# Kernel tuning notes

Measured on AMD Instinct MI355X. Metric: run time of the kernel, lower is better.

Reference implementation:

```python
import jax, jax.numpy as jnp
import numpy as np

N, E, D_IN, D_HID, D_OUT = 50000, 800000, 64, 128, 64


def setup_inputs() -> dict:
    key = jax.random.key(0)
    ks = jax.random.split(key, 8)
    x = jax.random.normal(ks[0], (N, D_IN), dtype=jnp.float32)
    edge_index = jax.random.randint(ks[1], (2, E), 0, N, dtype=jnp.int64)
    # SAGEConv layer 1: lin_l (agg path, with bias), lin_r (root path, no bias)
    s1 = 1.0 / np.sqrt(D_IN)
    W_l1 = jax.random.uniform(ks[2], (D_HID, D_IN), jnp.float32, -s1, s1)
    b_l1 = jnp.zeros((D_HID,), jnp.float32)
    W_r1 = jax.random.uniform(ks[3], (D_HID, D_IN), jnp.float32, -s1, s1)
    s2 = 1.0 / np.sqrt(D_HID)
    W_l2 = jax.random.uniform(ks[4], (D_OUT, D_HID), jnp.float32, -s2, s2)
    b_l2 = jnp.zeros((D_OUT,), jnp.float32)
    W_r2 = jax.random.uniform(ks[5], (D_OUT, D_HID), jnp.float32, -s2, s2)
    return {"x": x, "edge_index": edge_index,
            "W_l1": W_l1, "b_l1": b_l1, "W_r1": W_r1,
            "W_l2": W_l2, "b_l2": b_l2, "W_r2": W_r2}


def _sage_layer(h, src, dst, W_l, b_l, W_r, n_nodes):
    # scatter-mean of source features onto targets
    msg = h[src]                                               # [E, d]
    summed = jax.ops.segment_sum(msg, dst, num_segments=n_nodes)
    deg = jax.ops.segment_sum(jnp.ones((src.shape[0], 1), h.dtype), dst,
                              num_segments=n_nodes)
    agg = summed / jnp.maximum(deg, 1.0)                       # [n, d]
    return agg @ W_l.T + b_l + h @ W_r.T


def reference(x, edge_index, W_l1, b_l1, W_r1, W_l2, b_l2, W_r2):
    src, dst = edge_index[0], edge_index[1]
    n = x.shape[0]
    h = _sage_layer(x, src, dst, W_l1, b_l1, W_r1, n)
    h = jnp.tanh(h)
    h = _sage_layer(h, src, dst, W_l2, b_l2, W_r2, n)
    return jax.nn.log_softmax(h, axis=1)
```

## Files before the change

kernel.cpp:

```cpp
#include <hip/hip_runtime.h>
#include <hip/hip_bf16.h>
#include <math.h>


typedef unsigned short u16;
typedef unsigned int   u32;
typedef __attribute__((ext_vector_type(8))) __bf16 bf16x8;
typedef __attribute__((ext_vector_type(4))) float  f32x4;

__device__ __forceinline__ u16 f2bf(float f) {
    u32 u = __float_as_uint(f);
    u32 r = (u + 0x7FFFu + ((u >> 16) & 1u)) >> 16;
    return (u16)r;
}
__device__ __forceinline__ float bfl(u32 u) { return __uint_as_float(u << 16); }
__device__ __forceinline__ float bfh(u32 u) { return __uint_as_float(u & 0xFFFF0000u); }
__device__ __forceinline__ u32 pack2(float a, float b) {
    return (u32)f2bf(a) | ((u32)f2bf(b) << 16);
}
__device__ __forceinline__ int pad16(int x) { return (x + 15) & ~15; }

__global__ __launch_bounds__(256) void misc_kernel(
    const float* __restrict__ x, uint4* __restrict__ xb4, int nCvt8,
    const float* __restrict__ Wl1, const float* __restrict__ Wr1,
    const float* __restrict__ Wl2, const float* __restrict__ Wr2,
    u16* __restrict__ W1c, u16* __restrict__ W2c,
    u16* __restrict__ perm, int permStore8,
    int* __restrict__ cnt, int nCnt4,
    u16* __restrict__ xb, u16* __restrict__ m2b,
    int N, int VB, int PB, int ZB)
{
    int blk = blockIdx.x, tid = threadIdx.x;
    if (blk < VB) {
        int i = blk * 256 + tid;
        if (i < nCvt8) {
            float4 v0 = ((const float4*)x)[i * 2];
            float4 v1 = ((const float4*)x)[i * 2 + 1];
            uint4 p;
            p.x = pack2(v0.x, v0.y); p.y = pack2(v0.z, v0.w);
            p.z = pack2(v1.x, v1.y); p.w = pack2(v1.z, v1.w);
            xb4[i] = p;
        }
    } else if (blk < VB + 64) {
        int i = (blk - VB) * 256 + tid;
        if (i < 128 * 128) {
            int o = i >> 7, k = i & 127;
            float w1 = (k < 64) ? Wr1[o * 64 + k] : Wl1[o * 64 + (k - 64)];
            W1c[i] = f2bf(w1);
            float w2 = (o < 64) ? Wl2[o * 128 + k] : Wr2[(o - 64) * 128 + k];
            W2c[i] = f2bf(w2);
        }
    } else if (blk < VB + 64 + PB) {
        int i = (blk - VB - 64) * 256 + tid;
        if (i < permStore8) {
            u32 v = (u32)N | ((u32)N << 16);
            uint4 q; q.x = v; q.y = v; q.z = v; q.w = v;
            ((uint4*)perm)[i] = q;
        }
    } else if (blk < VB + 64 + PB + ZB) {
        int i = (blk - VB - 64 - PB) * 256 + tid;
        if (i < nCnt4) {
            uint4 z; z.x = 0; z.y = 0; z.z = 0; z.w = 0;
            ((uint4*)cnt)[i] = z;
        }
    } else {
        if (tid < 32)      ((u32*)(xb  + (size_t)N * 64))[tid] = 0;
        else if (tid < 64) ((u32*)(m2b + (size_t)N * 64))[tid - 32] = 0;
    }
}

__global__ __launch_bounds__(256) void fill_kernel(
    const int* __restrict__ src, const int* __restrict__ dst,
    int* __restrict__ cnt, u16* __restrict__ perm, int E, int N8, float invN8)
{
    int g = blockIdx.x & 7;
    int e0 = (blockIdx.x >> 3) * 2048 + threadIdx.x * 8;
    int d[8];
    if (e0 + 8 <= E) {
        int4 d0 = *(const int4*)(dst + e0);
        int4 d1 = *(const int4*)(dst + e0 + 4);
        d[0] = d0.x; d[1] = d0.y; d[2] = d0.z; d[3] = d0.w;
        d[4] = d1.x; d[5] = d1.y; d[6] = d1.z; d[7] = d1.w;
    } else {
        for (int k = 0; k < 8; k++) d[k] = (e0 + k < E) ? dst[e0 + k] : -1;
    }
#pragma unroll
    for (int k = 0; k < 8; k++) {
        int dd = d[k];
        if (dd < 0) continue;
        int b = (int)((float)dd * invN8);
        if (dd >= (b + 1) * N8) b++;
        else if (dd < b * N8) b--;
        if (b != g) continue;
        int pos = atomicAdd(&cnt[dd], 1);
        if (pos < 64) perm[(size_t)dd * 64 + pos] = (u16)src[e0 + k];
    }
}

__device__ __forceinline__ void gather_wide(
    const u32* __restrict__ feat2, const u16* __restrict__ perm,
    int slot0, int pd, int rg, int c8, float acc[8])
{
    float accB[8];
#pragma unroll
    for (int k = 0; k < 8; k++) { acc[k] = 0.f; accB[k] = 0.f; }
    int pidx = (int)perm[slot0 + (rg * 8 + c8)];
    for (int j = 0; j < pd; j += 16) {
        int rA = __shfl(pidx, j + rg,     64);
        int rB = __shfl(pidx, j + 8 + rg, 64);
        uint4 uA = *(const uint4*)(feat2 + (size_t)rA * 32 + c8 * 4);
        uint4 uB = *(const uint4*)(feat2 + (size_t)rB * 32 + c8 * 4);
        acc[0] += bfl(uA.x); acc[1] += bfh(uA.x);
        acc[2] += bfl(uA.y); acc[3] += bfh(uA.y);
        acc[4] += bfl(uA.z); acc[5] += bfh(uA.z);
        acc[6] += bfl(uA.w); acc[7] += bfh(uA.w);
        accB[0] += bfl(uB.x); accB[1] += bfh(uB.x);
        accB[2] += bfl(uB.y); accB[3] += bfh(uB.y);
        accB[4] += bfl(uB.z); accB[5] += bfh(uB.z);
        accB[6] += bfl(uB.w); accB[7] += bfh(uB.w);
    }
#pragma unroll
    for (int k = 0; k < 8; k++) acc[k] += accB[k];
#pragma unroll
    for (int k = 0; k < 8; k++) {
        acc[k] += __shfl_xor(acc[k], 8, 64);
        acc[k] += __shfl_xor(acc[k], 16, 64);
        acc[k] += __shfl_xor(acc[k], 32, 64);
    }
}

__global__ __launch_bounds__(256) void gather1_kernel(
    const u32* __restrict__ xb2, const u16* __restrict__ perm,
    const int* __restrict__ cnt, u32* __restrict__ aggb2, int N)
{
    int wid  = blockIdx.x * 4 + (threadIdx.x >> 6);
    int lane = threadIdx.x & 63;
    if (wid >= N) return;
    int deg = cnt[wid];
    int pd = pad16(min(deg, 64));
    int rg = lane >> 3, c8 = lane & 7;
    float acc[8];
    gather_wide(xb2, perm, wid * 64, pd, rg, c8, acc);
    if (rg == 0) {
        float inv = 1.f / fmaxf((float)deg, 1.f);
        uint4 p;
        p.x = pack2(acc[0] * inv, acc[1] * inv);
        p.y = pack2(acc[2] * inv, acc[3] * inv);
        p.z = pack2(acc[4] * inv, acc[5] * inv);
        p.w = pack2(acc[6] * inv, acc[7] * inv);
        *(uint4*)(aggb2 + (size_t)wid * 32 + c8 * 4) = p;
    }
}

__global__ __launch_bounds__(256) void layer12_mfma(
    const u16* __restrict__ xb, const u16* __restrict__ aggb,
    const u16* __restrict__ W1, const float* __restrict__ b1,
    const u16* __restrict__ W2, const float* __restrict__ b2,
    u16* __restrict__ m2b, float* __restrict__ out, int N)
{
    __shared__ u16 tile[4][2048];
    int tid = threadIdx.x;
    int wv = tid >> 6, lane = tid & 63;
    int quad = lane >> 4, l16 = lane & 15;
    int node = blockIdx.x * 64 + wv * 16 + l16;
    int nclamp = min(node, N - 1);
    const u16* xrow = xb   + (size_t)nclamp * 64;
    const u16* arow = aggb + (size_t)nclamp * 64;
    bf16x8 a0 = *(const bf16x8*)(xrow + quad * 8);
    bf16x8 a1 = *(const bf16x8*)(xrow + 32 + quad * 8);
    bf16x8 a2 = *(const bf16x8*)(arow + quad * 8);
    bf16x8 a3 = *(const bf16x8*)(arow + 32 + quad * 8);
#pragma unroll
    for (int nt = 0; nt < 8; nt++) {
        const u16* wrow = W1 + (size_t)(nt * 16 + l16) * 128 + quad * 8;
        f32x4 acc = {0.f, 0.f, 0.f, 0.f};
        acc = __builtin_amdgcn_mfma_f32_16x16x32_bf16(a0, *(const bf16x8*)(wrow),      acc, 0, 0, 0);
        acc = __builtin_amdgcn_mfma_f32_16x16x32_bf16(a1, *(const bf16x8*)(wrow + 32), acc, 0, 0, 0);
        acc = __builtin_amdgcn_mfma_f32_16x16x32_bf16(a2, *(const bf16x8*)(wrow + 64), acc, 0, 0, 0);
        acc = __builtin_amdgcn_mfma_f32_16x16x32_bf16(a3, *(const bf16x8*)(wrow + 96), acc, 0, 0, 0);
        int col = nt * 16 + l16;
        float bias = b1[col];
#pragma unroll
        for (int r = 0; r < 4; r++) {
            int row = quad * 4 + r;
            tile[wv][row * 128 + (col ^ ((row & 7) << 3))] =
                f2bf(tanhf(acc[r] + bias));
        }
    }
    __syncthreads();
    int swz = (l16 & 7) << 3;
    bf16x8 h0 = *(const bf16x8*)&tile[wv][l16 * 128 + (( 0 + quad * 8) ^ swz)];
    bf16x8 h1 = *(const bf16x8*)&tile[wv][l16 * 128 + ((32 + quad * 8) ^ swz)];
    bf16x8 h2 = *(const bf16x8*)&tile[wv][l16 * 128 + ((64 + quad * 8) ^ swz)];
    bf16x8 h3 = *(const bf16x8*)&tile[wv][l16 * 128 + ((96 + quad * 8) ^ swz)];
    int orow = blockIdx.x * 64 + wv * 16 + quad * 4;
#pragma unroll
    for (int nt = 0; nt < 8; nt++) {
        const u16* wrow = W2 + (size_t)(nt * 16 + l16) * 128 + quad * 8;
        f32x4 acc = {0.f, 0.f, 0.f, 0.f};
        acc = __builtin_amdgcn_mfma_f32_16x16x32_bf16(h0, *(const bf16x8*)(wrow),      acc, 0, 0, 0);
        acc = __builtin_amdgcn_mfma_f32_16x16x32_bf16(h1, *(const bf16x8*)(wrow + 32), acc, 0, 0, 0);
        acc = __builtin_amdgcn_mfma_f32_16x16x32_bf16(h2, *(const bf16x8*)(wrow + 64), acc, 0, 0, 0);
        acc = __builtin_amdgcn_mfma_f32_16x16x32_bf16(h3, *(const bf16x8*)(wrow + 96), acc, 0, 0, 0);
        int oc = nt * 16 + l16;
#pragma unroll
        for (int r = 0; r < 4; r++) {
            int nn = orow + r;
            if (nn >= N) continue;
            if (oc < 64) m2b[(size_t)nn * 64 + oc] = f2bf(acc[r]);
            else         out[(size_t)nn * 64 + (oc - 64)] = acc[r] + b2[oc - 64];
        }
    }
}

__global__ __launch_bounds__(256) void gather2_final_kernel(
    const u32* __restrict__ m2b2, const u16* __restrict__ perm,
    const int* __restrict__ cnt, float* __restrict__ out, int N)
{
    int wid  = blockIdx.x * 4 + (threadIdx.x >> 6);
    int lane = threadIdx.x & 63;
    if (wid >= N) return;
    int deg = cnt[wid];
    int pd = pad16(min(deg, 64));
    int rg = lane >> 3, c8 = lane & 7;
    float acc[8];
    gather_wide(m2b2, perm, wid * 64, pd, rg, c8, acc);
    float inv = 1.f / fmaxf((float)deg, 1.f);
    const float4* orow = (const float4*)(out + (size_t)wid * 64);
    float4 r20 = orow[c8 * 2];
    float4 r21 = orow[c8 * 2 + 1];
    float v[8];
    v[0] = acc[0] * inv + r20.x; v[1] = acc[1] * inv + r20.y;
    v[2] = acc[2] * inv + r20.z; v[3] = acc[3] * inv + r20.w;
    v[4] = acc[4] * inv + r21.x; v[5] = acc[5] * inv + r21.y;
    v[6] = acc[6] * inv + r21.z; v[7] = acc[7] * inv + r21.w;
    float m = v[0];
#pragma unroll
    for (int k = 1; k < 8; k++) m = fmaxf(m, v[k]);
#pragma unroll
    for (int o = 1; o < 8; o <<= 1) m = fmaxf(m, __shfl_xor(m, o, 64));
    float s = 0.f;
#pragma unroll
    for (int k = 0; k < 8; k++) s += expf(v[k] - m);
#pragma unroll
    for (int o = 1; o < 8; o <<= 1) s += __shfl_xor(s, o, 64);
    if (rg == 0) {
        float ls = m + logf(s);
        float4* ow = (float4*)(out + (size_t)wid * 64);
        ow[c8 * 2]     = make_float4(v[0] - ls, v[1] - ls, v[2] - ls, v[3] - ls);
        ow[c8 * 2 + 1] = make_float4(v[4] - ls, v[5] - ls, v[6] - ls, v[7] - ls);
    }
}

extern "C" void kernel_launch(void* const* d_in, const int* in_sizes, int n_in,
                              void* d_out, int out_size, void* d_ws, size_t ws_size,
                              hipStream_t stream)
{
    const float* x   = (const float*)d_in[0];
    const int*   ei  = (const int*)d_in[1];
    const float* Wl1 = (const float*)d_in[2];
    const float* bl1 = (const float*)d_in[3];
    const float* Wr1 = (const float*)d_in[4];
    const float* Wl2 = (const float*)d_in[5];
    const float* bl2 = (const float*)d_in[6];
    const float* Wr2 = (const float*)d_in[7];
    float* out = (float*)d_out;

    int N = in_sizes[0] / 64;
    int E = in_sizes[1] / 2;
    const int* src = ei;
    const int* dst = ei + E;
    int N8 = (N + 7) / 8;
    float invN8 = 1.0f / (float)N8;

    size_t permN = (size_t)N * 64;
    int permStore8 = (int)(permN / 8);
    int PB = (permStore8 + 255) / 256;

    char* wsb = (char*)d_ws;
    size_t npad = ((size_t)N + 64) & ~(size_t)63;
    int* cnt  = (int*)wsb;
    u16* perm = (u16*)(cnt + npad);
    u16* xb   = perm + permN;
    u16* aggb = xb + (size_t)(N + 1) * 64;
    u16* m2b  = aggb + (size_t)N * 64;
    u16* W1c  = m2b + (size_t)(N + 1) * 64;
    u16* W2c  = W1c + 128 * 128;

    int nCvt8 = N * 64 / 8;
    int VB = (nCvt8 + 255) / 256;
    int nCnt4 = N / 4;
    int ZB = (nCnt4 + 255) / 256;
    misc_kernel<<<VB + 64 + PB + ZB + 1, 256, 0, stream>>>(
        x, (uint4*)xb, nCvt8,
        Wl1, Wr1, Wl2, Wr2, W1c, W2c,
        perm, permStore8, cnt, nCnt4, xb, m2b, N, VB, PB, ZB);

    {
        int chunks = (E + 2047) / 2048;
        fill_kernel<<<chunks * 8, 256, 0, stream>>>(src, dst, cnt, perm, E,
                                                    N8, invN8);
    }

    gather1_kernel<<<(N + 3) / 4, 256, 0, stream>>>((const u32*)xb, perm,
                                                    cnt, (u32*)aggb, N);

    layer12_mfma<<<(N + 63) / 64, 256, 0, stream>>>(xb, aggb, W1c, bl1,
                                                    W2c, bl2, m2b, out, N);

    gather2_final_kernel<<<(N + 3) / 4, 256, 0, stream>>>((const u32*)m2b, perm,
                                                          cnt, out, N);
}
```

Baseline: 203.6 us.

## Fuse layer-1 gather into MFMA kernel and fold edge fill into prep

The layer-1 neighbor gather now runs inside the dense MFMA kernel. Eight waves gather 64 node rows into a swizzled LDS tile, then four waves run both layer matmuls on it, so the aggregated buffer no longer goes through global memory. The full perm prefill is dropped: lanes beyond a node's degree are masked to the zero sentinel row. The count reset is done with a memset, and the edge bucketing fill shares one launch with the x and weight bf16 conversions. The cost is that half the waves in the fused kernel sit idle during the matmul phase, and the block is larger, which may lower occupancy.

```diff
diff --git a/kernel.cpp b/kernel.cpp
--- a/kernel.cpp
+++ b/kernel.cpp
@@ -20,61 +20,13 @@
 }
 __device__ __forceinline__ int pad16(int x) { return (x + 15) & ~15; }
 
-__global__ __launch_bounds__(256) void misc_kernel(
-    const float* __restrict__ x, uint4* __restrict__ xb4, int nCvt8,
-    const float* __restrict__ Wl1, const float* __restrict__ Wr1,
-    const float* __restrict__ Wl2, const float* __restrict__ Wr2,
-    u16* __restrict__ W1c, u16* __restrict__ W2c,
-    u16* __restrict__ perm, int permStore8,
-    int* __restrict__ cnt, int nCnt4,
-    u16* __restrict__ xb, u16* __restrict__ m2b,
-    int N, int VB, int PB, int ZB)
-{
-    int blk = blockIdx.x, tid = threadIdx.x;
-    if (blk < VB) {
-        int i = blk * 256 + tid;
-        if (i < nCvt8) {
-            float4 v0 = ((const float4*)x)[i * 2];
-            float4 v1 = ((const float4*)x)[i * 2 + 1];
-            uint4 p;
-            p.x = pack2(v0.x, v0.y); p.y = pack2(v0.z, v0.w);
-            p.z = pack2(v1.x, v1.y); p.w = pack2(v1.z, v1.w);
-            xb4[i] = p;
-        }
-    } else if (blk < VB + 64) {
-        int i = (blk - VB) * 256 + tid;
-        if (i < 128 * 128) {
-            int o = i >> 7, k = i & 127;
-            float w1 = (k < 64) ? Wr1[o * 64 + k] : Wl1[o * 64 + (k - 64)];
-            W1c[i] = f2bf(w1);
-            float w2 = (o < 64) ? Wl2[o * 128 + k] : Wr2[(o - 64) * 128 + k];
-            W2c[i] = f2bf(w2);
-        }
-    } else if (blk < VB + 64 + PB) {
-        int i = (blk - VB - 64) * 256 + tid;
-        if (i < permStore8) {
-            u32 v = (u32)N | ((u32)N << 16);
-            uint4 q; q.x = v; q.y = v; q.z = v; q.w = v;
-            ((uint4*)perm)[i] = q;
-        }
-    } else if (blk < VB + 64 + PB + ZB) {
-        int i = (blk - VB - 64 - PB) * 256 + tid;
-        if (i < nCnt4) {
-            uint4 z; z.x = 0; z.y = 0; z.z = 0; z.w = 0;
-            ((uint4*)cnt)[i] = z;
-        }
-    } else {
-        if (tid < 32)      ((u32*)(xb  + (size_t)N * 64))[tid] = 0;
-        else if (tid < 64) ((u32*)(m2b + (size_t)N * 64))[tid - 32] = 0;
-    }
-}
-
-__global__ __launch_bounds__(256) void fill_kernel(
+__device__ __forceinline__ void fill_body(
     const int* __restrict__ src, const int* __restrict__ dst,
-    int* __restrict__ cnt, u16* __restrict__ perm, int E, int N8, float invN8)
-{
-    int g = blockIdx.x & 7;
-    int e0 = (blockIdx.x >> 3) * 2048 + threadIdx.x * 8;
+    int* __restrict__ cnt, u16* __restrict__ perm, int E, int N8,
+    float invN8, int vb, int tid)
+{
+    int g = vb & 7;
+    int e0 = (vb >> 3) * 2048 + tid * 8;
     int d[8];
     if (e0 + 8 <= E) {
         int4 d0 = *(const int4*)(dst + e0);
@@ -97,14 +49,54 @@
     }
 }
 
+__global__ __launch_bounds__(256) void prep_kernel(
+    const int* __restrict__ src, const int* __restrict__ dst,
+    int* __restrict__ cnt, u16* __restrict__ perm, int E, int N8, float invN8,
+    const float* __restrict__ x, uint4* __restrict__ xb4, int nCvt8,
+    const float* __restrict__ Wl1, const float* __restrict__ Wr1,
+    const float* __restrict__ Wl2, const float* __restrict__ Wr2,
+    u16* __restrict__ W1c, u16* __restrict__ W2c,
+    u16* __restrict__ xb, u16* __restrict__ m2b,
+    int N, int FB, int VB)
+{
+    int blk = blockIdx.x, tid = threadIdx.x;
+    if (blk < FB) {
+        fill_body(src, dst, cnt, perm, E, N8, invN8, blk, tid);
+    } else if (blk < FB + VB) {
+        int i = (blk - FB) * 256 + tid;
+        if (i < nCvt8) {
+            float4 v0 = ((const float4*)x)[i * 2];
+            float4 v1 = ((const float4*)x)[i * 2 + 1];
+            uint4 p;
+            p.x = pack2(v0.x, v0.y); p.y = pack2(v0.z, v0.w);
+            p.z = pack2(v1.x, v1.y); p.w = pack2(v1.z, v1.w);
+            xb4[i] = p;
+        }
+    } else if (blk < FB + VB + 64) {
+        int i = (blk - FB - VB) * 256 + tid;
+        if (i < 128 * 128) {
+            int o = i >> 7, k = i & 127;
+            float w1 = (k < 64) ? Wr1[o * 64 + k] : Wl1[o * 64 + (k - 64)];
+            W1c[i] = f2bf(w1);
+            float w2 = (o < 64) ? Wl2[o * 128 + k] : Wr2[(o - 64) * 128 + k];
+            W2c[i] = f2bf(w2);
+        }
+    } else {
+        if (tid < 32)      ((u32*)(xb  + (size_t)N * 64))[tid] = 0;
+        else if (tid < 64) ((u32*)(m2b + (size_t)N * 64))[tid - 32] = 0;
+    }
+}
+
 __device__ __forceinline__ void gather_wide(
     const u32* __restrict__ feat2, const u16* __restrict__ perm,
-    int slot0, int pd, int rg, int c8, float acc[8])
+    int slot0, int degc, int pd, int rg, int c8, int lane, int N,
+    float acc[8])
 {
     float accB[8];
 #pragma unroll
     for (int k = 0; k < 8; k++) { acc[k] = 0.f; accB[k] = 0.f; }
-    int pidx = (int)perm[slot0 + (rg * 8 + c8)];
+    int pidx = (int)perm[slot0 + lane];
+    pidx = (lane < degc) ? pidx : N;
     for (int j = 0; j < pd; j += 16) {
         int rA = __shfl(pidx, j + rg,     64);
         int rB = __shfl(pidx, j + 8 + rg, 64);
@@ -129,102 +121,116 @@
     }
 }
 
-__global__ __launch_bounds__(256) void gather1_kernel(
-    const u32* __restrict__ xb2, const u16* __restrict__ perm,
-    const int* __restrict__ cnt, u32* __restrict__ aggb2, int N)
+__global__ __launch_bounds__(512) void gather_layer12_kernel(
+    const u16* __restrict__ xb, const u16* __restrict__ perm,
+    const int* __restrict__ cnt,
+    const u16* __restrict__ W1, const float* __restrict__ b1,
+    const u16* __restrict__ W2, const float* __restrict__ b2,
+    u16* __restrict__ m2b, float* __restrict__ out, int N)
+{
+    __shared__ u16 agg_lds[64 * 64];
+    __shared__ u16 tile4[4 * 2048];
+    const int tid = threadIdx.x;
+    const int wv = tid >> 6, lane = tid & 63;
+    const int tb = blockIdx.x;
+
+    {
+        const int rg = lane >> 3, c8 = lane & 7;
+#pragma unroll 2
+        for (int i = 0; i < 8; i++) {
+            int rr = wv * 8 + i;
+            int nodec = min(tb * 64 + rr, N - 1);
+            int deg = cnt[nodec];
+            int degc = min(deg, 64);
+            int pd = pad16(degc);
+            float acc[8];
+            gather_wide((const u32*)xb, perm, nodec * 64, degc, pd,
+                        rg, c8, lane, N, acc);
+            if (rg == 0) {
+                float inv = 1.f / fmaxf((float)deg, 1.f);
+                uint4 p;
+                p.x = pack2(acc[0] * inv, acc[1] * inv);
+                p.y = pack2(acc[2] * inv, acc[3] * inv);
+                p.z = pack2(acc[4] * inv, acc[5] * inv);
+                p.w = pack2(acc[6] * inv, acc[7] * inv);
+                *(uint4*)&agg_lds[rr * 64 + ((c8 ^ (rr & 7)) << 3)] = p;
+            }
+        }
+    }
+    __syncthreads();
+
+    const int quad = lane >> 4, l16 = lane & 15;
+    u16* tile = tile4 + wv * 2048;
+    bf16x8 a0, a1, a2, a3;
+    if (wv < 4) {
+        int node = tb * 64 + wv * 16 + l16;
+        int nclamp = min(node, N - 1);
+        const u16* xrow = xb + (size_t)nclamp * 64;
+        a0 = *(const bf16x8*)(xrow + quad * 8);
+        a1 = *(const bf16x8*)(xrow + 32 + quad * 8);
+        int rr = wv * 16 + l16;
+        a2 = *(const bf16x8*)&agg_lds[rr * 64 + ((quad       ^ (rr & 7)) << 3)];
+        a3 = *(const bf16x8*)&agg_lds[rr * 64 + (((quad + 4) ^ (rr & 7)) << 3)];
+#pragma unroll
+        for (int nt = 0; nt < 8; nt++) {
+            const u16* wrow = W1 + (size_t)(nt * 16 + l16) * 128 + quad * 8;
+            f32x4 acc = {0.f, 0.f, 0.f, 0.f};
+            acc = __builtin_amdgcn_mfma_f32_16x16x32_bf16(a0, *(const bf16x8*)(wrow),      acc, 0, 0, 0);
+            acc = __builtin_amdgcn_mfma_f32_16x16x32_bf16(a1, *(const bf16x8*)(wrow + 32), acc, 0, 0, 0);
+            acc = __builtin_amdgcn_mfma_f32_16x16x32_bf16(a2, *(const bf16x8*)(wrow + 64), acc, 0, 0, 0);
+            acc = __builtin_amdgcn_mfma_f32_16x16x32_bf16(a3, *(const bf16x8*)(wrow + 96), acc, 0, 0, 0);
+            int col = nt * 16 + l16;
+            float bias = b1[col];
+#pragma unroll
+            for (int r = 0; r < 4; r++) {
+                int row = quad * 4 + r;
+                tile[row * 128 + (col ^ ((row & 7) << 3))] =
+                    f2bf(tanhf(acc[r] + bias));
+            }
+        }
+    }
+    __syncthreads();
+
+    if (wv < 4) {
+        int swz = (l16 & 7) << 3;
+        bf16x8 h0 = *(const bf16x8*)&tile[l16 * 128 + (( 0 + quad * 8) ^ swz)];
+        bf16x8 h1 = *(const bf16x8*)&tile[l16 * 128 + ((32 + quad * 8) ^ swz)];
+        bf16x8 h2 = *(const bf16x8*)&tile[l16 * 128 + ((64 + quad * 8) ^ swz)];
+        bf16x8 h3 = *(const bf16x8*)&tile[l16 * 128 + ((96 + quad * 8) ^ swz)];
+        int orow = tb * 64 + wv * 16 + quad * 4;
+#pragma unroll
+        for (int nt = 0; nt < 8; nt++) {
+            const u16* wrow = W2 + (size_t)(nt * 16 + l16) * 128 + quad * 8;
+            f32x4 acc = {0.f, 0.f, 0.f, 0.f};
+            acc = __builtin_amdgcn_mfma_f32_16x16x32_bf16(h0, *(const bf16x8*)(wrow),      acc, 0, 0, 0);
+            acc = __builtin_amdgcn_mfma_f32_16x16x32_bf16(h1, *(const bf16x8*)(wrow + 32), acc, 0, 0, 0);
+            acc = __builtin_amdgcn_mfma_f32_16x16x32_bf16(h2, *(const bf16x8*)(wrow + 64), acc, 0, 0, 0);
+            acc = __builtin_amdgcn_mfma_f32_16x16x32_bf16(h3, *(const bf16x8*)(wrow + 96), acc, 0, 0, 0);
+            int oc = nt * 16 + l16;
+#pragma unroll
+            for (int r = 0; r < 4; r++) {
+                int nn = orow + r;
+                if (nn >= N) continue;
+                if (oc < 64) m2b[(size_t)nn * 64 + oc] = f2bf(acc[r]);
+                else         out[(size_t)nn * 64 + (oc - 64)] = acc[r] + b2[oc - 64];
+            }
+        }
+    }
+}
+
+__global__ __launch_bounds__(256) void gather2_final_kernel(
+    const u32* __restrict__ m2b2, const u16* __restrict__ perm,
+    const int* __restrict__ cnt, float* __restrict__ out, int N)
 {
     int wid  = blockIdx.x * 4 + (threadIdx.x >> 6);
     int lane = threadIdx.x & 63;
     if (wid >= N) return;
     int deg = cnt[wid];
-    int pd = pad16(min(deg, 64));
+    int degc = min(deg, 64);
+    int pd = pad16(degc);
     int rg = lane >> 3, c8 = lane & 7;
     float acc[8];
-    gather_wide(xb2, perm, wid * 64, pd, rg, c8, acc);
-    if (rg == 0) {
-        float inv = 1.f / fmaxf((float)deg, 1.f);
-        uint4 p;
-        p.x = pack2(acc[0] * inv, acc[1] * inv);
-        p.y = pack2(acc[2] * inv, acc[3] * inv);
-        p.z = pack2(acc[4] * inv, acc[5] * inv);
-        p.w = pack2(acc[6] * inv, acc[7] * inv);
-        *(uint4*)(aggb2 + (size_t)wid * 32 + c8 * 4) = p;
-    }
-}
-
-__global__ __launch_bounds__(256) void layer12_mfma(
-    const u16* __restrict__ xb, const u16* __restrict__ aggb,
-    const u16* __restrict__ W1, const float* __restrict__ b1,
-    const u16* __restrict__ W2, const float* __restrict__ b2,
-    u16* __restrict__ m2b, float* __restrict__ out, int N)
-{
-    __shared__ u16 tile[4][2048];
-    int tid = threadIdx.x;
-    int wv = tid >> 6, lane = tid & 63;
-    int quad = lane >> 4, l16 = lane & 15;
-    int node = blockIdx.x * 64 + wv * 16 + l16;
-    int nclamp = min(node, N - 1);
-    const u16* xrow = xb   + (size_t)nclamp * 64;
-    const u16* arow = aggb + (size_t)nclamp * 64;
-    bf16x8 a0 = *(const bf16x8*)(xrow + quad * 8);
-    bf16x8 a1 = *(const bf16x8*)(xrow + 32 + quad * 8);
-    bf16x8 a2 = *(const bf16x8*)(arow + quad * 8);
-    bf16x8 a3 = *(const bf16x8*)(arow + 32 + quad * 8);
-#pragma unroll
-    for (int nt = 0; nt < 8; nt++) {
-        const u16* wrow = W1 + (size_t)(nt * 16 + l16) * 128 + quad * 8;
-        f32x4 acc = {0.f, 0.f, 0.f, 0.f};
-        acc = __builtin_amdgcn_mfma_f32_16x16x32_bf16(a0, *(const bf16x8*)(wrow),      acc, 0, 0, 0);
-        acc = __builtin_amdgcn_mfma_f32_16x16x32_bf16(a1, *(const bf16x8*)(wrow + 32), acc, 0, 0, 0);
-        acc = __builtin_amdgcn_mfma_f32_16x16x32_bf16(a2, *(const bf16x8*)(wrow + 64), acc, 0, 0, 0);
-        acc = __builtin_amdgcn_mfma_f32_16x16x32_bf16(a3, *(const bf16x8*)(wrow + 96), acc, 0, 0, 0);
-        int col = nt * 16 + l16;
-        float bias = b1[col];
-#pragma unroll
-        for (int r = 0; r < 4; r++) {
-            int row = quad * 4 + r;
-            tile[wv][row * 128 + (col ^ ((row & 7) << 3))] =
-                f2bf(tanhf(acc[r] + bias));
-        }
-    }
-    __syncthreads();
-    int swz = (l16 & 7) << 3;
-    bf16x8 h0 = *(const bf16x8*)&tile[wv][l16 * 128 + (( 0 + quad * 8) ^ swz)];
-    bf16x8 h1 = *(const bf16x8*)&tile[wv][l16 * 128 + ((32 + quad * 8) ^ swz)];
-    bf16x8 h2 = *(const bf16x8*)&tile[wv][l16 * 128 + ((64 + quad * 8) ^ swz)];
-    bf16x8 h3 = *(const bf16x8*)&tile[wv][l16 * 128 + ((96 + quad * 8) ^ swz)];
-    int orow = blockIdx.x * 64 + wv * 16 + quad * 4;
-#pragma unroll
-    for (int nt = 0; nt < 8; nt++) {
-        const u16* wrow = W2 + (size_t)(nt * 16 + l16) * 128 + quad * 8;
-        f32x4 acc = {0.f, 0.f, 0.f, 0.f};
-        acc = __builtin_amdgcn_mfma_f32_16x16x32_bf16(h0, *(const bf16x8*)(wrow),      acc, 0, 0, 0);
-        acc = __builtin_amdgcn_mfma_f32_16x16x32_bf16(h1, *(const bf16x8*)(wrow + 32), acc, 0, 0, 0);
-        acc = __builtin_amdgcn_mfma_f32_16x16x32_bf16(h2, *(const bf16x8*)(wrow + 64), acc, 0, 0, 0);
-        acc = __builtin_amdgcn_mfma_f32_16x16x32_bf16(h3, *(const bf16x8*)(wrow + 96), acc, 0, 0, 0);
-        int oc = nt * 16 + l16;
-#pragma unroll
-        for (int r = 0; r < 4; r++) {
-            int nn = orow + r;
-            if (nn >= N) continue;
-            if (oc < 64) m2b[(size_t)nn * 64 + oc] = f2bf(acc[r]);
-            else         out[(size_t)nn * 64 + (oc - 64)] = acc[r] + b2[oc - 64];
-        }
-    }
-}
-
-__global__ __launch_bounds__(256) void gather2_final_kernel(
-    const u32* __restrict__ m2b2, const u16* __restrict__ perm,
-    const int* __restrict__ cnt, float* __restrict__ out, int N)
-{
-    int wid  = blockIdx.x * 4 + (threadIdx.x >> 6);
-    int lane = threadIdx.x & 63;
-    if (wid >= N) return;
-    int deg = cnt[wid];
-    int pd = pad16(min(deg, 64));
-    int rg = lane >> 3, c8 = lane & 7;
-    float acc[8];
-    gather_wide(m2b2, perm, wid * 64, pd, rg, c8, acc);
+    gather_wide(m2b2, perm, wid * 64, degc, pd, rg, c8, lane, N, acc);
     float inv = 1.f / fmaxf((float)deg, 1.f);
     const float4* orow = (const float4*)(out + (size_t)wid * 64);
     float4 r20 = orow[c8 * 2];
@@ -272,42 +278,31 @@
     const int* dst = ei + E;
     int N8 = (N + 7) / 8;
     float invN8 = 1.0f / (float)N8;
-
-    size_t permN = (size_t)N * 64;
-    int permStore8 = (int)(permN / 8);
-    int PB = (permStore8 + 255) / 256;
+    int chunks = (E + 2047) / 2048;
+    int FB = chunks * 8;
+    int nCvt8 = N * 64 / 8;
+    int VB = (nCvt8 + 255) / 256;
 
     char* wsb = (char*)d_ws;
     size_t npad = ((size_t)N + 64) & ~(size_t)63;
+    size_t permN = (size_t)N * 64;
     int* cnt  = (int*)wsb;
     u16* perm = (u16*)(cnt + npad);
     u16* xb   = perm + permN;
-    u16* aggb = xb + (size_t)(N + 1) * 64;
-    u16* m2b  = aggb + (size_t)N * 64;
+    u16* m2b  = xb + (size_t)(N + 1) * 64;
     u16* W1c  = m2b + (size_t)(N + 1) * 64;
     u16* W2c  = W1c + 128 * 128;
 
-    int nCvt8 = N * 64 / 8;
-    int VB = (nCvt8 + 255) / 256;
-    int nCnt4 = N / 4;
-    int ZB = (nCnt4 + 255) / 256;
-    misc_kernel<<<VB + 64 + PB + ZB + 1, 256, 0, stream>>>(
+    hipMemsetAsync(cnt, 0, (size_t)N * sizeof(int), stream);
+
+    prep_kernel<<<FB + VB + 64 + 1, 256, 0, stream>>>(
+        src, dst, cnt, perm, E, N8, invN8,
         x, (uint4*)xb, nCvt8,
-        Wl1, Wr1, Wl2, Wr2, W1c, W2c,
-        perm, permStore8, cnt, nCnt4, xb, m2b, N, VB, PB, ZB);
-
-    {
-        int chunks = (E + 2047) / 2048;
-        fill_kernel<<<chunks * 8, 256, 0, stream>>>(src, dst, cnt, perm, E,
-                                                    N8, invN8);
-    }
-
-    gather1_kernel<<<(N + 3) / 4, 256, 0, stream>>>((const u32*)xb, perm,
-                                                    cnt, (u32*)aggb, N);
-
-    layer12_mfma<<<(N + 63) / 64, 256, 0, stream>>>(xb, aggb, W1c, bl1,
-                                                    W2c, bl2, m2b, out, N);
-
-    gather2_final_kernel<<<(N + 3) / 4, 256, 0, stream>>>((const u32*)m2b, perm,
-                                                          cnt, out, N);
-}
+        Wl1, Wr1, Wl2, Wr2, W1c, W2c, xb, m2b, N, FB, VB);
+
+    gather_layer12_kernel<<<(N + 63) / 64, 512, 0, stream>>>(
+        xb, perm, cnt, W1c, bl1, W2c, bl2, m2b, out, N);
+
+    gather2_final_kernel<<<(N + 3) / 4, 256, 0, stream>>>(
+        (const u32*)m2b, perm, cnt, out, N);
+}
```

New measurement: 199.0 us, median of 2. 1.02x faster.
